# Kernel tuning notes

Hardware: AMD Instinct MI355X
Metric: run time of the kernel (lower is better)

The kernel has to match this reference:

```python
import jax, jax.numpy as jnp
import numpy as np

B, C, D, H, W = 4, 1, 192, 192, 192
SMALL = 4            # int(192 * bias_scale=0.025)
BIAS_STD = 0.7
MAX_SIGMA = 3.0
TRUNCATE = 4.0
K = 2 * int(TRUNCATE * MAX_SIGMA) + 1   # fixed truncated kernel size = 25
N_LABELS = 32
TABLE = 128          # static remap-table size (>= max source label, >= max dest)


def setup_inputs() -> dict:
    key = jax.random.key(0)
    k1, k2, k3, k4, k5 = jax.random.split(key, 5)
    return {
        "x": jax.random.normal(k1, (B, C, D, H, W), jnp.float32),
        "small_bias": jax.random.normal(k2, (B, 1, SMALL, SMALL, SMALL), jnp.float32),
        "sigma01": jax.random.uniform(k3, (B, 3), jnp.float32),
        "labels": jax.random.randint(k4, (B, 1, D, H, W), 0, N_LABELS, jnp.int32),
        "source_values": jnp.arange(N_LABELS, dtype=jnp.int64),
        "dest_values": jax.random.randint(k5, (N_LABELS,), 0, 100, jnp.int64),
    }


def _lin_weights(n_in, n_out):
    """Dense 1D linear-interp matrix [n_out, n_in], align_corners=True."""
    pos = jnp.linspace(0.0, n_in - 1.0, n_out)
    i0 = jnp.clip(jnp.floor(pos).astype(jnp.int32), 0, n_in - 2)
    f = pos - i0.astype(pos.dtype)
    r = jnp.arange(n_out)
    Wm = jnp.zeros((n_out, n_in), jnp.float32)
    Wm = Wm.at[r, i0].add(1.0 - f).at[r, i0 + 1].add(f)
    return Wm


def _bias_field(small_bias):
    # trilinear align_corners upsample [B,1,s,s,s] -> [B,1,D,H,W], separable
    b = small_bias * BIAS_STD
    b = jnp.einsum('bcxyz,dx->bcdyz', b, _lin_weights(SMALL, D))
    b = jnp.einsum('bcdyz,hy->bcdhz', b, _lin_weights(SMALL, H))
    b = jnp.einsum('bcdhz,wz->bcdhw', b, _lin_weights(SMALL, W))
    return b


def _gauss_kernels(sigma):
    """sigma [3] -> normalized kernels [3, K]; identity (delta) where sigma<0.01."""
    ar = jnp.arange(K, dtype=jnp.float32) - K // 2
    s = jnp.maximum(sigma, 1e-3)[:, None]
    g = jnp.exp(-0.5 * (ar[None, :] ** 2) / (s ** 2))
    g = g / g.sum(-1, keepdims=True)
    delta = jnp.zeros((K,), jnp.float32).at[K // 2].set(1.0)
    return jnp.where(sigma[:, None] >= 0.01, g, delta[None, :])


def _blur_axis(x, k, axis):
    # x [C,D,H,W]; depthwise 1D conv along `axis` with replicate (edge) padding
    p = K // 2
    xm = jnp.moveaxis(x, axis, -1)
    shp = xm.shape
    xm = xm.reshape(-1, 1, shp[-1])
    xm = jnp.pad(xm, ((0, 0), (0, 0), (p, p)), mode='edge')
    out = jax.lax.conv_general_dilated(xm, k.reshape(1, 1, K), (1,), 'VALID')
    return jnp.moveaxis(out.reshape(shp), -1, axis)


def _blur_sample(x, kernels):
    # x [C,D,H,W], kernels [3,K]; separable blur over D,H,W
    for i, ax in enumerate((1, 2, 3)):
        x = _blur_axis(x, kernels[i], ax)
    return x


def reference(x, small_bias, sigma01, labels, source_values, dest_values):
    # 1) bias-field corruption: x * exp(upsampled random field)
    img = x * jnp.exp(_bias_field(small_bias))
    # 2) dynamic per-sample Gaussian blur, sigma in [0, MAX_SIGMA]
    kernels = jax.vmap(_gauss_kernels)(sigma01 * MAX_SIGMA)   # [B,3,K]
    img = jax.vmap(_blur_sample)(img, kernels)
    # 3) label remap via lookup table gather
    mapping = jnp.zeros((TABLE,), jnp.int32).at[source_values].set(
        dest_values.astype(jnp.int32))
    labels_out = mapping[labels]
    return img, labels_out
```

## Files before the change

kernel.cpp:

```cpp
#include <hip/hip_runtime.h>
#include <hip/hip_fp16.h>
#include <cstdint>
#include <cstddef>

#define Bc 4
#define Dd 192
#define Hh 192
#define Ww 192
#define KK 25
#define RR 12
#define VOL (Bc*Dd*Hh*Ww)
#define SP 216
#define SPU (SP/2)
#define SH 98
#define RIN 88

typedef unsigned short u16;
typedef unsigned int   u32;

__global__ void setup_tables_kernel(const float* __restrict__ sigma01,
                                    const int* __restrict__ src,
                                    const int* __restrict__ dst,
                                    float* __restrict__ kern,
                                    u32* __restrict__ kern2,
                                    int* __restrict__ mapping,
                                    float* __restrict__ mapf) {
    int t = threadIdx.x;
    if (t < 128) mapping[t] = 0;
    __syncthreads();
    if (t < 32) {
        int s = src[t];
        if (s >= 0 && s < 128) mapping[s] = dst[t];
    }
    __syncthreads();
    if (t < 128) mapf[t] = (float)mapping[t];
    if (t < Bc * 3) {
        float sig = sigma01[t] * 3.0f;
        float s = fmaxf(sig, 1e-3f);
        float g[KK];
        float sum = 0.0f;
        #pragma unroll
        for (int i = 0; i < KK; i++) {
            float a = (float)(i - RR);
            float v = expf(-0.5f * a * a / (s * s));
            g[i] = v; sum += v;
        }
        float inv = 1.0f / sum;
        #pragma unroll
        for (int i = 0; i < KK; i++) {
            float v = g[i] * inv;
            if (sig < 0.01f) v = (i == RR) ? 1.0f : 0.0f;
            kern[t * KK + i] = v;
            u16 hb = __builtin_bit_cast(u16, __float2half(v));
            kern2[t * KK + i] = (u32)hb | ((u32)hb << 16);
        }
    }
}

__global__ __launch_bounds__(256) void pass_wh_kernel(
    const float* __restrict__ x, u16* __restrict__ outB,
    const u32* __restrict__ kern2,
    const float* __restrict__ sb) {
    __shared__ u16 P[RIN * SP];
    __shared__ __attribute__((aligned(16))) float ch[RIN][4];
    const int tid = threadIdx.x;
    const int hx = blockIdx.x;
    const int d  = blockIdx.y;
    const int b  = blockIdx.z;

    if (tid < RIN) {
        int r = tid;
        int hrow = min(max(64 * hx - RR + r, 0), Hh - 1);
        float pos_d = d * (3.0f / 191.0f);
        int   id0   = min((int)pos_d, 2);
        float fd    = pos_d - (float)id0;
        float pos_h = hrow * (3.0f / 191.0f);
        int   ih0   = min((int)pos_h, 2);
        float fh    = pos_h - (float)ih0;
        const float* sbA = sb + b * 64 + id0 * 16 + ih0 * 4;
        #pragma unroll
        for (int k = 0; k < 4; k++) {
            float v00 = sbA[k],      v01 = sbA[4 + k];
            float v10 = sbA[16 + k], v11 = sbA[20 + k];
            float vd0 = (1.f - fd) * v00 + fd * v10;
            float vd1 = (1.f - fd) * v01 + fd * v11;
            ch[r][k] = ((1.f - fh) * vd0 + fh * vd1) * 0.7f;
        }
    }
    __syncthreads();

    const size_t pbase = ((size_t)b * Dd + d) * (size_t)(Hh * Ww);
    #pragma unroll
    for (int it = 0; it < 17; it++) {
        int i4 = it * 256 + tid;
        if (i4 < RIN * 48) {
            int r = i4 / 48, w4 = i4 % 48;
            int w = 4 * w4;
            int hrow = min(max(64 * hx - RR + r, 0), Hh - 1);
            float4 v = *(const float4*)(x + pbase + (size_t)hrow * Ww + w);
            float4 cv = *(const float4*)&ch[r][0];
            float rs[4];
            #pragma unroll
            for (int j = 0; j < 4; j++) {
                float pw = (w + j) * (3.0f / 191.0f);
                bool s1 = pw >= 1.0f, s2 = pw >= 2.0f;
                float clo = s2 ? cv.z : (s1 ? cv.y : cv.x);
                float chi = s2 ? cv.w : (s1 ? cv.z : cv.y);
                float fb  = s2 ? 2.0f : (s1 ? 1.0f : 0.0f);
                float fw  = pw - fb;
                float bias = clo + fw * (chi - clo);
                float val = (j == 0 ? v.x : j == 1 ? v.y : j == 2 ? v.z : v.w);
                rs[j] = val * __expf(bias);
            }
            u32 p0 = (u32)__builtin_bit_cast(u16, __float2half(rs[0])) |
                     ((u32)__builtin_bit_cast(u16, __float2half(rs[1])) << 16);
            u32 p1 = (u32)__builtin_bit_cast(u16, __float2half(rs[2])) |
                     ((u32)__builtin_bit_cast(u16, __float2half(rs[3])) << 16);
            u32* dstp = (u32*)&P[r * SP + RR + w];
            dstp[0] = p0; dstp[1] = p1;
            if (w4 == 0) {
                u16 hv = __builtin_bit_cast(u16, __float2half(rs[0]));
                u32 hh = (u32)hv | ((u32)hv << 16);
                u32* hp = (u32*)&P[r * SP];
                #pragma unroll
                for (int m = 0; m < 6; m++) hp[m] = hh;
            } else if (w4 == 47) {
                u16 hv = __builtin_bit_cast(u16, __float2half(rs[3]));
                u32 hh = (u32)hv | ((u32)hv << 16);
                u32* hp = (u32*)&P[r * SP + RR + Ww];
                #pragma unroll
                for (int m = 0; m < 6; m++) hp[m] = hh;
            }
        }
    }
    __syncthreads();

    {
        const u32* kw2 = kern2 + (b * 3 + 2) * KK;
        const int wv = tid >> 6, ln = tid & 63;
        const int r4 = ln >> 4;
        const int c  = ln & 15;
        #pragma unroll
        for (int it = 0; it < 6; it++) {
            const int lr = it * 4 + r4;
            if (lr < 22) {
                const int row = wv * 22 + lr;
                const u32* rp = (const u32*)P + row * SPU + 6 * c;
                u32 E[18];
                #pragma unroll
                for (int j = 0; j < 18; j++) E[j] = rp[j];
                u32 O[17];
                #pragma unroll
                for (int j = 0; j < 17; j++)
                    O[j] = (E[j] >> 16) | (E[j + 1] << 16);
                __half2 acc[6];
                #pragma unroll
                for (int m = 0; m < 6; m++) acc[m] = __float2half2_rn(0.0f);
                #pragma unroll
                for (int s = 0; s < 13; s++) {
                    __half2 kv = __builtin_bit_cast(__half2, kw2[2 * s]);
                    #pragma unroll
                    for (int m = 0; m < 6; m++)
                        acc[m] = __hfma2(kv, __builtin_bit_cast(__half2, E[m + s]), acc[m]);
                }
                #pragma unroll
                for (int s = 0; s < 12; s++) {
                    __half2 kv = __builtin_bit_cast(__half2, kw2[2 * s + 1]);
                    #pragma unroll
                    for (int m = 0; m < 6; m++)
                        acc[m] = __hfma2(kv, __builtin_bit_cast(__half2, O[m + s]), acc[m]);
                }
                u32* wp = (u32*)P + row * SPU + 6 + 6 * c;
                #pragma unroll
                for (int m = 0; m < 6; m++)
                    wp[m] = __builtin_bit_cast(u32, acc[m]);
            }
        }
    }
    __syncthreads();

    {
        const u32* kh2 = kern2 + (b * 3 + 1) * KK;
        u32* outp = (u32*)(outB + pbase);
        #pragma unroll
        for (int it = 0; it < 3; it++) {
            int item = it * 256 + tid;
            int col = item % 96;
            int g = item / 96;
            u32 win[32];
            #pragma unroll
            for (int i = 0; i < 32; i++)
                win[i] = *((const u32*)P + (g * 8 + i) * SPU + 6 + col);
            __half2 acc[8];
            #pragma unroll
            for (int j = 0; j < 8; j++) acc[j] = __float2half2_rn(0.0f);
            #pragma unroll
            for (int t = 0; t < KK; t++) {
                __half2 kv = __builtin_bit_cast(__half2, kh2[t]);
                #pragma unroll
                for (int j = 0; j < 8; j++)
                    acc[j] = __hfma2(kv, __builtin_bit_cast(__half2, win[j + t]), acc[j]);
            }
            #pragma unroll
            for (int j = 0; j < 8; j++)
                outp[(64 * hx + g * 8 + j) * 96 + col] =
                    __builtin_bit_cast(u32, acc[j]);
        }
    }
}

__global__ __launch_bounds__(192) void pass_d_remap_kernel(
    const u16* __restrict__ in, float* __restrict__ img,
    const u32* __restrict__ kern2,
    const int4* __restrict__ labels, float4* __restrict__ lab_out,
    const float* __restrict__ mapf) {
    __shared__ __attribute__((aligned(16))) u16 T[88 * SH];
    __shared__ float Lmap[128];
    const int tid = threadIdx.x;
    const int w0 = blockIdx.x * 96;
    const int d0 = blockIdx.y * 64;
    const int z = blockIdx.z;
    const int h = z % Hh, b = z / Hh;
    const u32* kp = kern2 + b * 3 * KK;
    if (tid < 128) Lmap[tid] = mapf[tid];
    #pragma unroll
    for (int k = 0; k < 6; k++) {
        int idx = k * 192 + tid;
        if (idx < 1056) {
            int r = idx / 12, sg = idx % 12;
            int dd = min(max(d0 + r - RR, 0), Dd - 1);
            uint4 v = *(const uint4*)(in + (((size_t)b * Dd + dd) * Hh + h) * (size_t)Ww + w0 + sg * 8);
            u32* p = (u32*)&T[r * SH + sg * 8];
            p[0] = v.x; p[1] = v.y; p[2] = v.z; p[3] = v.w;
        }
    }
    __syncthreads();
    const int p = tid % 48;
    const int g0 = tid / 48;
    #pragma unroll
    for (int cc = 0; cc < 2; cc++) {
        const int g = g0 + cc * 4;
        const int ob = g * 8;
        u32 win[32];
        #pragma unroll
        for (int i = 0; i < 32; i++) win[i] = *(const u32*)&T[(ob + i) * SH + 2 * p];
        __half2 acc[8];
        #pragma unroll
        for (int j = 0; j < 8; j++) acc[j] = __float2half2_rn(0.0f);
        #pragma unroll
        for (int t = 0; t < KK; t++) {
            __half2 kv = __builtin_bit_cast(__half2, kp[t]);
            #pragma unroll
            for (int j = 0; j < 8; j++)
                acc[j] = __hfma2(kv, __builtin_bit_cast(__half2, win[j + t]), acc[j]);
        }
        #pragma unroll
        for (int j = 0; j < 8; j++) {
            float2 f = __half22float2(acc[j]);
            *(float2*)(img + (((size_t)b * Dd + (d0 + ob + j)) * Hh + h) * (size_t)Ww + w0 + 2 * p) = f;
        }
    }
    {
        const int bid = (z * 3 + blockIdx.y) * 2 + blockIdx.x;
        int base = bid * 1536 + tid;
        #pragma unroll
        for (int it = 0; it < 8; it++) {
            int i = base + it * 192;
            int4 l = labels[i];
            float4 o;
            o.x = Lmap[min(max(l.x, 0), 127)];
            o.y = Lmap[min(max(l.y, 0), 127)];
            o.z = Lmap[min(max(l.z, 0), 127)];
            o.w = Lmap[min(max(l.w, 0), 127)];
            lab_out[i] = o;
        }
    }
}

extern "C" void kernel_launch(void* const* d_in, const int* in_sizes, int n_in,
                              void* d_out, int out_size, void* d_ws, size_t ws_size,
                              hipStream_t stream) {
    const float* x          = (const float*)d_in[0];
    const float* small_bias = (const float*)d_in[1];
    const float* sigma01    = (const float*)d_in[2];
    const int*   labels     = (const int*)d_in[3];
    const int*   src        = (const int*)d_in[4];
    const int*   dst        = (const int*)d_in[5];

    float* out     = (float*)d_out;
    float* img     = out;
    float* lab_out = out + (size_t)VOL;

    float* kern    = (float*)d_ws;
    u32*   kern2   = (u32*)((float*)d_ws + 384);
    int*   mapping = (int*)((float*)d_ws + 768);
    float* mapf    = (float*)d_ws + 896;
    u16*   Bb      = (u16*)((char*)d_ws + 8192);

    setup_tables_kernel<<<1, 128, 0, stream>>>(sigma01, src, dst, kern, kern2,
                                               mapping, mapf);

    pass_wh_kernel<<<dim3(3, Dd, Bc), 256, 0, stream>>>(x, Bb, kern2, small_bias);
    pass_d_remap_kernel<<<dim3(Ww / 96, Dd / 64, Bc * Hh), 192, 0, stream>>>(
        Bb, img, kern2, (const int4*)labels, (float4*)lab_out, mapf);
}
```

Measured before the change: 154.1 us.

## Move label remap into W/H blur pass and streamline bias and fp16 packing

Moves the label remap out of the depth-pass kernel and into the W/H blur kernel. Label loads are issued before the convolution compute so their latency overlaps the ALU work, and the remapped results are stored afterwards, with the table read directly from global memory. The bias interpolation is rewritten to store precomputed (value, slope) pairs and index them instead of chaining selects. fp16 packing now uses cvt_pkrtz (round-toward-zero instead of round-to-nearest), and native half2 vector arithmetic replaces __hfma2. Holding 12 int4 label registers across the compute phase, plus the launch_bounds occupancy hint, raises register pressure and may cause spills.

```diff
diff --git a/kernel.cpp b/kernel.cpp
--- a/kernel.cpp
+++ b/kernel.cpp
@@ -17,11 +17,15 @@
 
 typedef unsigned short u16;
 typedef unsigned int   u32;
+typedef __fp16 h2 __attribute__((ext_vector_type(2)));
+
+__device__ inline u32 pk2(float a, float b) {
+    return __builtin_bit_cast(u32, __builtin_amdgcn_cvt_pkrtz(a, b));
+}
 
 __global__ void setup_tables_kernel(const float* __restrict__ sigma01,
                                     const int* __restrict__ src,
                                     const int* __restrict__ dst,
-                                    float* __restrict__ kern,
                                     u32* __restrict__ kern2,
                                     int* __restrict__ mapping,
                                     float* __restrict__ mapf) {
@@ -50,19 +54,19 @@
         for (int i = 0; i < KK; i++) {
             float v = g[i] * inv;
             if (sig < 0.01f) v = (i == RR) ? 1.0f : 0.0f;
-            kern[t * KK + i] = v;
             u16 hb = __builtin_bit_cast(u16, __float2half(v));
             kern2[t * KK + i] = (u32)hb | ((u32)hb << 16);
         }
     }
 }
 
-__global__ __launch_bounds__(256) void pass_wh_kernel(
+__global__ __launch_bounds__(256, 4) void pass_wh_remap_kernel(
     const float* __restrict__ x, u16* __restrict__ outB,
-    const u32* __restrict__ kern2,
-    const float* __restrict__ sb) {
+    const u32* __restrict__ kern2, const float* __restrict__ sb,
+    const int4* __restrict__ labels, float4* __restrict__ lab_out,
+    const float* __restrict__ mapf) {
     __shared__ u16 P[RIN * SP];
-    __shared__ __attribute__((aligned(16))) float ch[RIN][4];
+    __shared__ float2 ch2[RIN * 3];
     const int tid = threadIdx.x;
     const int hx = blockIdx.x;
     const int d  = blockIdx.y;
@@ -78,14 +82,18 @@
         int   ih0   = min((int)pos_h, 2);
         float fh    = pos_h - (float)ih0;
         const float* sbA = sb + b * 64 + id0 * 16 + ih0 * 4;
+        float c[4];
         #pragma unroll
         for (int k = 0; k < 4; k++) {
             float v00 = sbA[k],      v01 = sbA[4 + k];
             float v10 = sbA[16 + k], v11 = sbA[20 + k];
             float vd0 = (1.f - fd) * v00 + fd * v10;
             float vd1 = (1.f - fd) * v01 + fd * v11;
-            ch[r][k] = ((1.f - fh) * vd0 + fh * vd1) * 0.7f;
-        }
+            c[k] = ((1.f - fh) * vd0 + fh * vd1) * 0.7f;
+        }
+        #pragma unroll
+        for (int k = 0; k < 3; k++)
+            ch2[r * 3 + k] = make_float2(c[k], c[k + 1] - c[k]);
     }
     __syncthreads();
 
@@ -98,35 +106,26 @@
             int w = 4 * w4;
             int hrow = min(max(64 * hx - RR + r, 0), Hh - 1);
             float4 v = *(const float4*)(x + pbase + (size_t)hrow * Ww + w);
-            float4 cv = *(const float4*)&ch[r][0];
             float rs[4];
             #pragma unroll
             for (int j = 0; j < 4; j++) {
-                float pw = (w + j) * (3.0f / 191.0f);
-                bool s1 = pw >= 1.0f, s2 = pw >= 2.0f;
-                float clo = s2 ? cv.z : (s1 ? cv.y : cv.x);
-                float chi = s2 ? cv.w : (s1 ? cv.z : cv.y);
-                float fb  = s2 ? 2.0f : (s1 ? 1.0f : 0.0f);
-                float fw  = pw - fb;
-                float bias = clo + fw * (chi - clo);
+                float pw = (float)(w + j) * (3.0f / 191.0f);
+                int sel = (pw >= 1.0f) + (pw >= 2.0f);
+                float2 cd = ch2[r * 3 + sel];
+                float bias = fmaf(pw - (float)sel, cd.y, cd.x);
                 float val = (j == 0 ? v.x : j == 1 ? v.y : j == 2 ? v.z : v.w);
                 rs[j] = val * __expf(bias);
             }
-            u32 p0 = (u32)__builtin_bit_cast(u16, __float2half(rs[0])) |
-                     ((u32)__builtin_bit_cast(u16, __float2half(rs[1])) << 16);
-            u32 p1 = (u32)__builtin_bit_cast(u16, __float2half(rs[2])) |
-                     ((u32)__builtin_bit_cast(u16, __float2half(rs[3])) << 16);
             u32* dstp = (u32*)&P[r * SP + RR + w];
-            dstp[0] = p0; dstp[1] = p1;
+            dstp[0] = pk2(rs[0], rs[1]);
+            dstp[1] = pk2(rs[2], rs[3]);
             if (w4 == 0) {
-                u16 hv = __builtin_bit_cast(u16, __float2half(rs[0]));
-                u32 hh = (u32)hv | ((u32)hv << 16);
+                u32 hh = pk2(rs[0], rs[0]);
                 u32* hp = (u32*)&P[r * SP];
                 #pragma unroll
                 for (int m = 0; m < 6; m++) hp[m] = hh;
             } else if (w4 == 47) {
-                u16 hv = __builtin_bit_cast(u16, __float2half(rs[3]));
-                u32 hh = (u32)hv | ((u32)hv << 16);
+                u32 hh = pk2(rs[3], rs[3]);
                 u32* hp = (u32*)&P[r * SP + RR + Ww];
                 #pragma unroll
                 for (int m = 0; m < 6; m++) hp[m] = hh;
@@ -134,6 +133,13 @@
         }
     }
     __syncthreads();
+
+    const int bid = (b * Dd + d) * 3 + hx;
+    const int4* lp = labels + (size_t)bid * 3072 + tid;
+    int4 lab[12];
+    #pragma unroll
+    for (int m = 0; m < 12; m++) lab[m] = lp[m * 256];
+    __builtin_amdgcn_sched_barrier(0);
 
     {
         const u32* kw2 = kern2 + (b * 3 + 2) * KK;
@@ -153,22 +159,22 @@
                 #pragma unroll
                 for (int j = 0; j < 17; j++)
                     O[j] = (E[j] >> 16) | (E[j + 1] << 16);
-                __half2 acc[6];
-                #pragma unroll
-                for (int m = 0; m < 6; m++) acc[m] = __float2half2_rn(0.0f);
+                h2 acc[6];
+                #pragma unroll
+                for (int m = 0; m < 6; m++) acc[m] = (h2)(0.0f);
                 #pragma unroll
                 for (int s = 0; s < 13; s++) {
-                    __half2 kv = __builtin_bit_cast(__half2, kw2[2 * s]);
+                    h2 kv = __builtin_bit_cast(h2, kw2[2 * s]);
                     #pragma unroll
                     for (int m = 0; m < 6; m++)
-                        acc[m] = __hfma2(kv, __builtin_bit_cast(__half2, E[m + s]), acc[m]);
+                        acc[m] += kv * __builtin_bit_cast(h2, E[m + s]);
                 }
                 #pragma unroll
                 for (int s = 0; s < 12; s++) {
-                    __half2 kv = __builtin_bit_cast(__half2, kw2[2 * s + 1]);
+                    h2 kv = __builtin_bit_cast(h2, kw2[2 * s + 1]);
                     #pragma unroll
                     for (int m = 0; m < 6; m++)
-                        acc[m] = __hfma2(kv, __builtin_bit_cast(__half2, O[m + s]), acc[m]);
+                        acc[m] += kv * __builtin_bit_cast(h2, O[m + s]);
                 }
                 u32* wp = (u32*)P + row * SPU + 6 + 6 * c;
                 #pragma unroll
@@ -191,15 +197,15 @@
             #pragma unroll
             for (int i = 0; i < 32; i++)
                 win[i] = *((const u32*)P + (g * 8 + i) * SPU + 6 + col);
-            __half2 acc[8];
-            #pragma unroll
-            for (int j = 0; j < 8; j++) acc[j] = __float2half2_rn(0.0f);
+            h2 acc[8];
+            #pragma unroll
+            for (int j = 0; j < 8; j++) acc[j] = (h2)(0.0f);
             #pragma unroll
             for (int t = 0; t < KK; t++) {
-                __half2 kv = __builtin_bit_cast(__half2, kh2[t]);
+                h2 kv = __builtin_bit_cast(h2, kh2[t]);
                 #pragma unroll
                 for (int j = 0; j < 8; j++)
-                    acc[j] = __hfma2(kv, __builtin_bit_cast(__half2, win[j + t]), acc[j]);
+                    acc[j] += kv * __builtin_bit_cast(h2, win[j + t]);
             }
             #pragma unroll
             for (int j = 0; j < 8; j++)
@@ -207,22 +213,32 @@
                     __builtin_bit_cast(u32, acc[j]);
         }
     }
-}
-
-__global__ __launch_bounds__(192) void pass_d_remap_kernel(
+
+    {
+        float4* op = lab_out + (size_t)bid * 3072 + tid;
+        #pragma unroll
+        for (int m = 0; m < 12; m++) {
+            int4 l = lab[m];
+            float4 o;
+            o.x = mapf[min(max(l.x, 0), 127)];
+            o.y = mapf[min(max(l.y, 0), 127)];
+            o.z = mapf[min(max(l.z, 0), 127)];
+            o.w = mapf[min(max(l.w, 0), 127)];
+            op[m * 256] = o;
+        }
+    }
+}
+
+__global__ __launch_bounds__(192) void pass_d_kernel(
     const u16* __restrict__ in, float* __restrict__ img,
-    const u32* __restrict__ kern2,
-    const int4* __restrict__ labels, float4* __restrict__ lab_out,
-    const float* __restrict__ mapf) {
+    const u32* __restrict__ kern2) {
     __shared__ __attribute__((aligned(16))) u16 T[88 * SH];
-    __shared__ float Lmap[128];
     const int tid = threadIdx.x;
     const int w0 = blockIdx.x * 96;
     const int d0 = blockIdx.y * 64;
     const int z = blockIdx.z;
     const int h = z % Hh, b = z / Hh;
     const u32* kp = kern2 + b * 3 * KK;
-    if (tid < 128) Lmap[tid] = mapf[tid];
     #pragma unroll
     for (int k = 0; k < 6; k++) {
         int idx = k * 192 + tid;
@@ -244,35 +260,21 @@
         u32 win[32];
         #pragma unroll
         for (int i = 0; i < 32; i++) win[i] = *(const u32*)&T[(ob + i) * SH + 2 * p];
-        __half2 acc[8];
-        #pragma unroll
-        for (int j = 0; j < 8; j++) acc[j] = __float2half2_rn(0.0f);
+        h2 acc[8];
+        #pragma unroll
+        for (int j = 0; j < 8; j++) acc[j] = (h2)(0.0f);
         #pragma unroll
         for (int t = 0; t < KK; t++) {
-            __half2 kv = __builtin_bit_cast(__half2, kp[t]);
+            h2 kv = __builtin_bit_cast(h2, kp[t]);
             #pragma unroll
             for (int j = 0; j < 8; j++)
-                acc[j] = __hfma2(kv, __builtin_bit_cast(__half2, win[j + t]), acc[j]);
+                acc[j] += kv * __builtin_bit_cast(h2, win[j + t]);
         }
         #pragma unroll
         for (int j = 0; j < 8; j++) {
-            float2 f = __half22float2(acc[j]);
+            h2 a = acc[j];
+            float2 f = make_float2((float)a.x, (float)a.y);
             *(float2*)(img + (((size_t)b * Dd + (d0 + ob + j)) * Hh + h) * (size_t)Ww + w0 + 2 * p) = f;
-        }
-    }
-    {
-        const int bid = (z * 3 + blockIdx.y) * 2 + blockIdx.x;
-        int base = bid * 1536 + tid;
-        #pragma unroll
-        for (int it = 0; it < 8; it++) {
-            int i = base + it * 192;
-            int4 l = labels[i];
-            float4 o;
-            o.x = Lmap[min(max(l.x, 0), 127)];
-            o.y = Lmap[min(max(l.y, 0), 127)];
-            o.z = Lmap[min(max(l.z, 0), 127)];
-            o.w = Lmap[min(max(l.w, 0), 127)];
-            lab_out[i] = o;
         }
     }
 }
@@ -291,16 +293,16 @@
     float* img     = out;
     float* lab_out = out + (size_t)VOL;
 
-    float* kern    = (float*)d_ws;
     u32*   kern2   = (u32*)((float*)d_ws + 384);
     int*   mapping = (int*)((float*)d_ws + 768);
     float* mapf    = (float*)d_ws + 896;
     u16*   Bb      = (u16*)((char*)d_ws + 8192);
 
-    setup_tables_kernel<<<1, 128, 0, stream>>>(sigma01, src, dst, kern, kern2,
+    setup_tables_kernel<<<1, 128, 0, stream>>>(sigma01, src, dst, kern2,
                                                mapping, mapf);
 
-    pass_wh_kernel<<<dim3(3, Dd, Bc), 256, 0, stream>>>(x, Bb, kern2, small_bias);
-    pass_d_remap_kernel<<<dim3(Ww / 96, Dd / 64, Bc * Hh), 192, 0, stream>>>(
-        Bb, img, kern2, (const int4*)labels, (float4*)lab_out, mapf);
-}
+    pass_wh_remap_kernel<<<dim3(3, Dd, Bc), 256, 0, stream>>>(
+        x, Bb, kern2, small_bias,
+        (const int4*)labels, (float4*)lab_out, mapf);
+    pass_d_kernel<<<dim3(Ww / 96, Dd / 64, Bc * Hh), 192, 0, stream>>>(Bb, img, kern2);
+}
```

Result: faster. 143.6 us (-6.9%).
